# Kernel optimization log

Hardware: AMD Instinct MI355X
Metric: run time of the kernel (lower is better)

## Reference

```python
import jax, jax.numpy as jnp
import numpy as np

IN_C, OUT_C, K, PAD = 4, 32, 5, 2
B, H, W = 128, 84, 84
T_MAX = 15.0
BASE_THR = 15.0
TARGET_RATE = 0.05
LR_PLUS, LR_MINUS = 0.004, 0.0012
HOMEO, EMA_DECAY = 0.01, 0.99
FAN_IN_SQRT = float((IN_C * K * K) ** 0.5)


def setup_inputs() -> dict:
    key = jax.random.key(0)
    k1, k2, k3 = jax.random.split(key, 3)
    lat = jax.random.uniform(k1, (B, IN_C, H, W), jnp.float32, 0.0, T_MAX)
    lat = lat * (jax.random.uniform(k3, (B, IN_C, H, W)) > 0.3).astype(jnp.float32)
    w = jax.random.uniform(k2, (OUT_C, IN_C, K, K)) * 0.6 + 0.2
    norm = jnp.linalg.norm(w.reshape(OUT_C, -1), axis=1).reshape(-1, 1, 1, 1)
    w = w / (norm + 1e-6) * FAN_IN_SQRT
    thr = jnp.full((OUT_C,), BASE_THR, jnp.float32)
    ema = jnp.full((OUT_C,), TARGET_RATE, jnp.float32)
    return {"spike_latencies": lat, "weight": w, "adaptive_threshold": thr, "firing_rate_ema": ema}


def reference(spike_latencies, weight, adaptive_threshold, firing_rate_ema):
    # is_training_stdp=True path: returns (out_latencies, new_weight, new_threshold, new_ema)
    active = (spike_latencies > 0).astype(spike_latencies.dtype)   # (B,Cin,H,W)
    pot_in = (T_MAX - spike_latencies) * active
    pot_out = jax.lax.conv_general_dilated(
        pot_in, weight, (1, 1), [(PAD, PAD), (PAD, PAD)],
        dimension_numbers=("NCHW", "OIHW", "NCHW"))                # (B,Cout,H,W)

    winners = jnp.argmax(pot_out, axis=1)                           # (B,H,W)
    max_pot = jnp.max(pot_out, axis=1)                              # (B,H,W)
    win_thr = adaptive_threshold[winners]                           # (B,H,W)
    fire = (max_pot >= win_thr).astype(pot_out.dtype)               # (B,H,W)
    out_spikes = jax.nn.one_hot(winners, OUT_C, axis=1, dtype=pot_out.dtype) * fire[:, None]

    winners_flat = winners.reshape(-1)                              # (N,) N = B*H*W
    fire_flat = fire.reshape(-1)

    # ---- homeostatic threshold update (no_grad in torch) ----
    count = jax.ops.segment_sum(fire_flat, winners_flat, num_segments=OUT_C)  # fires per channel
    spatial_count = float(B * H * W)
    cur_rate = count / (spatial_count + 1e-8)
    new_ema = EMA_DECAY * firing_rate_ema + (1.0 - EMA_DECAY) * cur_rate
    rate_err = new_ema - TARGET_RATE
    new_thr = jnp.clip(adaptive_threshold + HOMEO * rate_err * adaptive_threshold,
                       BASE_THR * 0.1, BASE_THR * 5.0)

    # ---- STDP weight update (no_grad in torch) ----
    # im2col of the binary activity map; feature dim is ordered (Cin, K, K)
    patches = jax.lax.conv_general_dilated_patches(
        active, (K, K), (1, 1), [(PAD, PAD), (PAD, PAD)])           # (B, Cin*K*K, H, W)
    patches = patches.transpose(0, 2, 3, 1).reshape(-1, IN_C, K, K)  # (N,Cin,K,K)

    # sum of pre-activity patches per winning channel, masked by fire
    S_pre = jax.ops.segment_sum(patches * fire_flat[:, None, None, None],
                                winners_flat, num_segments=OUT_C)    # (Cout,Cin,K,K)

    fired = count > 0
    # min/max over the gathered winner weights == min/max over channels that fired
    ch_min = weight.min(axis=(1, 2, 3))
    ch_max = weight.max(axis=(1, 2, 3))
    w_min = jnp.min(jnp.where(fired, ch_min, jnp.inf))
    w_max = jnp.max(jnp.where(fired, ch_max, -jnp.inf))
    w_normed = (weight - w_min) / (w_max - w_min + 1e-6)

    # sum over fired positions of per-position delta, closed form per channel
    cnt = count[:, None, None, None]
    total_delta = LR_PLUS * (1.0 - w_normed) * S_pre - LR_MINUS * w_normed * (cnt - S_pre)
    total_delta = jnp.where(fired[:, None, None, None],
                            total_delta / jnp.maximum(cnt, 1.0), 0.0)

    w_upd = jnp.maximum(weight + total_delta, 0.01)
    norm = jnp.linalg.norm(w_upd.reshape(OUT_C, -1), axis=1).reshape(-1, 1, 1, 1)
    w_upd = w_upd / (norm + 1e-6) * FAN_IN_SQRT
    new_weight = jnp.where(jnp.any(fired), w_upd, weight)

    out_latencies = (T_MAX * BASE_THR / (max_pot + 1e-5))[:, None] * out_spikes  # (B,Cout,H,W)
    return out_latencies, new_weight, new_thr, new_ema
```

## Files before the change

### kernel.cpp

```cpp
#include <hip/hip_runtime.h>
#include <hip/hip_bf16.h>

#define H_ 84
#define W_ 84
#define B_ 128
#define ICN 4
#define OCN 32
#define HW (H_*W_)
#define OUT_LAT (B_*OCN*HW)
#define OUT_WOFF OUT_LAT
#define OUT_THROFF (OUT_WOFF + 3200)
#define OUT_EMAOFF (OUT_WOFF + 3232)

#define WF_OFF   0
#define SPRE_OFF 903168
#define CNT_OFF  (SPRE_OFF + 12800)
#define LCNT_OFF (CNT_OFF + 128)
#define W4T_OFF  (LCNT_OFF + 128)
#define LIST_OFF (W4T_OFF + 12800)
#define LIST_CAP 32768
#define PART_OFF (LIST_OFF + LIST_CAP*4)
#define NSLAB 7
#define NBLK (B_*NSLAB)
#define LREDN 3232

__global__ __launch_bounds__(256) void wtrans_kernel(const float* __restrict__ w,
                                                     float* __restrict__ w4t) {
  int i = blockIdx.x * 256 + threadIdx.x;
  if (i < 3200) {
    int c = i / 100, r = i % 100, ic = r / 25, t = r % 25;
    w4t[(t * 32 + c) * 4 + ic] = w[i];
  }
}

__global__ __launch_bounds__(256, 4) void conv_kernel(const float* __restrict__ lat,
    const float* __restrict__ w4t, const float* __restrict__ thr,
    float* __restrict__ out, unsigned char* __restrict__ wfmap,
    unsigned* __restrict__ lcnt, unsigned* __restrict__ list) {
  __shared__ float4 tile[20][20];
  const int b = blockIdx.z;
  const int bx = blockIdx.x * 16, by = blockIdx.y * 16;
  const int tid = threadIdx.y * 16 + threadIdx.x;
  const float* base = lat + (size_t)b * ICN * HW;
  for (int n = tid; n < 400; n += 256) {
    int iy = n / 20, ix = n % 20;
    int gy = by + iy - 2, gx = bx + ix - 2;
    float4 v = make_float4(0.f, 0.f, 0.f, 0.f);
    if (gy >= 0 && gy < H_ && gx >= 0 && gx < W_) {
      const float* p = base + gy * W_ + gx;
      float a0 = p[0], a1 = p[HW], a2 = p[2 * HW], a3 = p[3 * HW];
      v.x = a0 > 0.f ? 15.0f - a0 : 0.f;
      v.y = a1 > 0.f ? 15.0f - a1 : 0.f;
      v.z = a2 > 0.f ? 15.0f - a2 : 0.f;
      v.w = a3 > 0.f ? 15.0f - a3 : 0.f;
    }
    tile[iy][ix] = v;
  }
  __syncthreads();
  const int x = bx + threadIdx.x, y = by + threadIdx.y;
  if (x >= W_ || y >= H_) return;
  const float4* w4 = (const float4*)w4t;
  float s[32];
  #pragma unroll
  for (int c = 0; c < 32; c++) s[c] = 0.f;
  for (int i = 0; i < 5; i++) {
    for (int j = 0; j < 5; j++) {
      float4 pv = tile[threadIdx.y + i][threadIdx.x + j];
      int t = i * 5 + j;
      #pragma unroll
      for (int c = 0; c < 32; c++) {
        float4 wv = w4[t * 32 + c];
        s[c] = fmaf(pv.x, wv.x, s[c]);
        s[c] = fmaf(pv.y, wv.y, s[c]);
        s[c] = fmaf(pv.z, wv.z, s[c]);
        s[c] = fmaf(pv.w, wv.w, s[c]);
      }
    }
  }
  float best = s[0], second = -__builtin_inff();
  int bc = 0, bc2 = 0;
  #pragma unroll
  for (int c = 1; c < 32; c++) {
    float v = s[c];
    if (v > best) { second = best; bc2 = bc; best = v; bc = c; }
    else if (v > second) { second = v; bc2 = c; }
  }
  float tb = thr[bc];
  bool fire = best >= tb;
  float latv = 225.0f / (best + 1e-5f);
  bool risky_gap = (best - second) < 0.02f;
  bool risky_thr = fabsf(best - tb) < 0.02f;
  bool need_exact = risky_thr || (risky_gap && latv >= 0.55f);
  bool deferred = false;
  if (need_exact) {
    unsigned idx = atomicAdd(lcnt, 1u);
    if (idx < LIST_CAP) { list[idx] = (unsigned)(b * HW + y * W_ + x); deferred = true; }
  }
  if (!deferred) {
    bool split = risky_gap && !need_exact;
    wfmap[b * HW + y * W_ + x] = (unsigned char)(bc | (fire ? 0x80 : 0));
    if (fire) {
      size_t o = (size_t)b * OCN * HW + (size_t)y * W_ + x;
      if (split) {
        float h = 0.5f * latv;
        out[o + (size_t)bc  * HW] = h;
        out[o + (size_t)bc2 * HW] = h;
      } else {
        out[o + (size_t)bc * HW] = latv;
      }
    }
  }
}

__global__ __launch_bounds__(256, 2) void repair_kernel(const float* __restrict__ lat,
    const float* __restrict__ weight, const float* __restrict__ thr,
    float* __restrict__ out, unsigned char* __restrict__ wfmap,
    const unsigned* __restrict__ lcnt, const unsigned* __restrict__ list) {
  unsigned n = *lcnt;
  if (n > LIST_CAP) n = LIST_CAP;
  for (unsigned i = blockIdx.x * 256 + threadIdx.x; i < n; i += gridDim.x * 256) {
    unsigned pix = list[i];
    int b = (int)(pix / HW), r = (int)(pix % HW);
    int y = r / W_, x = r % W_;
    const float* base = lat + (size_t)b * ICN * HW;
    float raw[100];
    #pragma unroll
    for (int ic = 0; ic < 4; ic++)
      #pragma unroll
      for (int kh = 0; kh < 5; kh++)
        #pragma unroll
        for (int kw = 0; kw < 5; kw++) {
          int gy = y + kh - 2, gx = x + kw - 2;
          raw[ic * 25 + kh * 5 + kw] =
            (gy >= 0 && gy < H_ && gx >= 0 && gx < W_) ? base[ic * HW + gy * W_ + gx] : 0.f;
        }
    double dbest = -1.0e300;
    int bc = 0;
    for (int c = 0; c < 32; c++) {
      const float* wr = weight + c * 100;
      double s = 0.0;
      for (int q = 0; q < 100; q++) {
        float a = raw[q];
        double pot = a > 0.f ? 15.0 - (double)a : 0.0;
        s += pot * (double)wr[q];
      }
      if (s > dbest) { dbest = s; bc = c; }
    }
    bool fire = dbest >= (double)thr[bc];
    wfmap[pix] = (unsigned char)(bc | (fire ? 0x80 : 0));
    if (fire)
      out[((size_t)b * OCN + bc) * HW + (size_t)y * W_ + x] = (float)(225.0 / (dbest + 1e-5));
  }
}

__device__ __forceinline__ unsigned long long winshift(unsigned long long lo,
                                                       unsigned long long hi, int s) {
  if (s < 0)  return lo << (-s);
  if (s == 0) return lo;
  if (s < 64) return (lo >> s) | (hi << (64 - s));
  return hi >> (s - 64);
}

__global__ __launch_bounds__(256, 4) void spre_kernel(const float* __restrict__ lat,
    const unsigned char* __restrict__ wfmap,
    unsigned* __restrict__ spre, unsigned* __restrict__ cnt,
    unsigned* __restrict__ partial) {
  __shared__ unsigned arow[16][ICN][3];
  __shared__ unsigned lred[LREDN];
  const int b = blockIdx.x;
  const int y0 = blockIdx.y * 12;
  const int tid = threadIdx.x;
  const int wv = tid >> 6, lane = tid & 63;
  for (int i = tid; i < LREDN; i += 256) lred[i] = 0;
  #pragma unroll
  for (int i = 0; i < 16; i++) {
    int pair = wv * 16 + i;
    int r = pair >> 2, ic = pair & 3;
    int gy = y0 - 2 + r;
    unsigned w0 = 0, w1 = 0, w2 = 0;
    if (gy >= 0 && gy < H_) {
      const float* rp = lat + ((size_t)b * ICN + ic) * HW + gy * W_;
      unsigned long long mA = __ballot(rp[lane] > 0.f);
      float vB = (lane < 20) ? rp[64 + lane] : 0.f;
      unsigned long long mB = __ballot(vB > 0.f);
      w0 = (unsigned)mA; w1 = (unsigned)(mA >> 32); w2 = (unsigned)mB;
    }
    if (lane == 0) { arow[r][ic][0] = w0; arow[r][ic][1] = w1; arow[r][ic][2] = w2; }
  }
  __syncthreads();
  unsigned acc0[16], acc1[16];
  #pragma unroll
  for (int c = 0; c < 16; c++) { acc0[c] = 0; acc1[c] = 0; }
  for (int k = 0; k < 6; k++) {
    int task = k * 4 + wv;
    int y = y0 + (task >> 1);
    int grp = task & 1;
    int xbase = grp * 64;
    bool valid = (grp == 0) || (lane < 20);
    unsigned wf = valid ? (unsigned)wfmap[b * HW + y * W_ + xbase + lane] : 0u;
    bool f = valid && (wf & 0x80u);
    int wc = (int)(wf & 31u);
    unsigned long long win0, win1;
    {
      int q = lane;
      int ic = q / 25, rr = q % 25, kh = rr / 5, kw = rr % 5;
      int ry = (y - y0) + kh;
      unsigned a0 = arow[ry][ic][0], a1 = arow[ry][ic][1], a2 = arow[ry][ic][2];
      unsigned long long lo = ((unsigned long long)a1 << 32) | a0;
      unsigned long long hi = a2;
      win0 = winshift(lo, hi, xbase + kw - 2);
      if (lane < 36) {
        q = 64 + lane;
        ic = q / 25; rr = q % 25; kh = rr / 5; kw = rr % 5;
        ry = (y - y0) + kh;
        a0 = arow[ry][ic][0]; a1 = arow[ry][ic][1]; a2 = arow[ry][ic][2];
        lo = ((unsigned long long)a1 << 32) | a0; hi = a2;
        win1 = winshift(lo, hi, xbase + kw - 2);
      } else if (lane == 36) {
        win1 = grp ? ((1ull << 20) - 1) : ~0ull;
      } else {
        win1 = 0ull;
      }
    }
    #pragma unroll
    for (int cc = 0; cc < 16; cc++) {
      unsigned long long m0 = __ballot(f && (wc == cc));
      unsigned long long m1 = __ballot(f && (wc == 16 + cc));
      acc0[cc] += (unsigned)__popcll(win0 & m0) | ((unsigned)__popcll(win0 & m1) << 16);
      acc1[cc] += (unsigned)__popcll(win1 & m0) | ((unsigned)__popcll(win1 & m1) << 16);
    }
  }
  #pragma unroll
  for (int cc = 0; cc < 16; cc++) {
    atomicAdd(&lred[cc * 101 + lane], acc0[cc] & 0xFFFFu);
    atomicAdd(&lred[(cc + 16) * 101 + lane], acc0[cc] >> 16);
    if (lane <= 36) {
      int q = (lane < 36) ? 64 + lane : 100;
      atomicAdd(&lred[cc * 101 + q], acc1[cc] & 0xFFFFu);
      atomicAdd(&lred[(cc + 16) * 101 + q], acc1[cc] >> 16);
    }
  }
  __syncthreads();
  if (partial) {
    unsigned bflat = (unsigned)(blockIdx.x * NSLAB + blockIdx.y);
    for (int i = tid; i < LREDN; i += 256)
      partial[bflat * LREDN + i] = lred[i];
  } else {
    for (int i = tid; i < LREDN; i += 256) {
      unsigned v = lred[i];
      if (v) {
        int c = i / 101, q = i % 101;
        if (q < 100) atomicAdd(&spre[c * 100 + q], v);
        else         atomicAdd(&cnt[c], v);
      }
    }
  }
}

__global__ __launch_bounds__(256) void reduce_kernel(const unsigned* __restrict__ partial,
    unsigned* __restrict__ spre, unsigned* __restrict__ cnt) {
  int i = blockIdx.x * 256 + threadIdx.x;
  if (i >= LREDN) return;
  unsigned s = 0;
  for (int j = 0; j < NBLK; j++) s += partial[(size_t)j * LREDN + i];
  int c = i / 101, q = i % 101;
  if (q < 100) spre[c * 100 + q] = s;
  else         cnt[c] = s;
}

__global__ void finalize_kernel(const float* __restrict__ weight, const float* __restrict__ thr,
    const float* __restrict__ ema, const unsigned* __restrict__ spre,
    const unsigned* __restrict__ cnt, float* __restrict__ out) {
  int lane = threadIdx.x;
  int c = lane & 31;
  bool hold = lane < 32;
  unsigned cu = cnt[c];
  float cntf = (float)cu;
  bool fired = cu > 0u;
  float emaN = 0.99f * ema[c] + 0.01f * (cntf / (903168.0f + 1e-8f));
  float thrN = thr[c] + 0.01f * (emaN - 0.05f) * thr[c];
  thrN = fminf(fmaxf(thrN, 1.5f), 75.0f);
  float chmin = __builtin_inff(), chmax = -__builtin_inff();
  for (int j = 0; j < 100; j++) {
    float w = weight[c * 100 + j];
    chmin = fminf(chmin, w); chmax = fmaxf(chmax, w);
  }
  float vmin = (hold && fired) ? chmin : __builtin_inff();
  float vmax = (hold && fired) ? chmax : -__builtin_inff();
  #pragma unroll
  for (int o = 1; o < 64; o <<= 1) {
    vmin = fminf(vmin, __shfl_xor(vmin, o));
    vmax = fmaxf(vmax, __shfl_xor(vmax, o));
  }
  bool any = __ballot(hold && fired) != 0ull;
  float denom = vmax - vmin + 1e-6f;
  float invc = 1.0f / fmaxf(cntf, 1.0f);
  float sumsq = 0.f;
  for (int j = 0; j < 100; j++) {
    float w = weight[c * 100 + j];
    float wn = (w - vmin) / denom;
    float sp = (float)spre[c * 100 + j];
    float d = 0.004f * (1.0f - wn) * sp - 0.0012f * wn * (cntf - sp);
    d = fired ? d * invc : 0.0f;
    float wu = fmaxf(w + d, 0.01f);
    sumsq += wu * wu;
  }
  float scale = 10.0f / (sqrtf(sumsq) + 1e-6f);
  if (hold) {
    for (int j = 0; j < 100; j++) {
      float w = weight[c * 100 + j];
      float wn = (w - vmin) / denom;
      float sp = (float)spre[c * 100 + j];
      float d = 0.004f * (1.0f - wn) * sp - 0.0012f * wn * (cntf - sp);
      d = fired ? d * invc : 0.0f;
      float wu = fmaxf(w + d, 0.01f);
      out[OUT_WOFF + c * 100 + j] = any ? wu * scale : w;
    }
    out[OUT_THROFF + c] = thrN;
    out[OUT_EMAOFF + c] = emaN;
  }
}

extern "C" void kernel_launch(void* const* d_in, const int* in_sizes, int n_in,
                              void* d_out, int out_size, void* d_ws, size_t ws_size,
                              hipStream_t stream) {
  (void)in_sizes; (void)n_in; (void)out_size;
  const float* lat    = (const float*)d_in[0];
  const float* weight = (const float*)d_in[1];
  const float* thr    = (const float*)d_in[2];
  const float* ema    = (const float*)d_in[3];
  float* out = (float*)d_out;
  char* ws = (char*)d_ws;
  unsigned char* wfmap = (unsigned char*)(ws + WF_OFF);
  unsigned* spre = (unsigned*)(ws + SPRE_OFF);
  unsigned* cnt  = (unsigned*)(ws + CNT_OFF);
  unsigned* lcnt = (unsigned*)(ws + LCNT_OFF);
  float* w4t     = (float*)(ws + W4T_OFF);
  unsigned* list = (unsigned*)(ws + LIST_OFF);
  unsigned* part = (unsigned*)(ws + PART_OFF);
  bool useP = ws_size >= (size_t)PART_OFF + (size_t)NBLK * LREDN * 4;

  hipMemsetAsync(d_out, 0, (size_t)OUT_LAT * 4, stream);
  hipMemsetAsync(ws + SPRE_OFF, 0, 12800 + 256, stream);
  wtrans_kernel<<<13, 256, 0, stream>>>(weight, w4t);
  conv_kernel<<<dim3(6, 6, B_), dim3(16, 16, 1), 0, stream>>>(lat, w4t, thr, out, wfmap, lcnt, list);
  repair_kernel<<<64, 256, 0, stream>>>(lat, weight, thr, out, wfmap, lcnt, list);
  spre_kernel<<<dim3(B_, NSLAB), 256, 0, stream>>>(lat, wfmap, spre, cnt, useP ? part : nullptr);
  if (useP) reduce_kernel<<<(LREDN + 255) / 256, 256, 0, stream>>>(part, spre, cnt);
  finalize_kernel<<<1, 64, 0, stream>>>(weight, thr, ema, spre, cnt, out);
}
```

Measured before the change: 275.4 us.

## Cache input patch in registers and loop over output channels with streaming argmax

Reorders the convolution loops so each thread loads its 5x5x4 input patch from shared memory into registers once. It then iterates over output channels, computing one dot product at a time and updating the running top-two argmax as it goes, instead of keeping 32 accumulators live. The transposed weights are re-laid out channel-major to match this order, and the shared tile row is padded to 21 to reduce bank conflicts. The cost is about 100 VGPRs for the patch and long serial FMA chains with only 2-way channel unrolling, which risks spills or less latency hiding under the 256x4 launch bounds.

```diff
diff --git a/kernel.cpp b/kernel.cpp
--- a/kernel.cpp
+++ b/kernel.cpp
@@ -29,7 +29,7 @@
   int i = blockIdx.x * 256 + threadIdx.x;
   if (i < 3200) {
     int c = i / 100, r = i % 100, ic = r / 25, t = r % 25;
-    w4t[(t * 32 + c) * 4 + ic] = w[i];
+    w4t[(c * 25 + t) * 4 + ic] = w[i];
   }
 }
 
@@ -37,7 +37,7 @@
     const float* __restrict__ w4t, const float* __restrict__ thr,
     float* __restrict__ out, unsigned char* __restrict__ wfmap,
     unsigned* __restrict__ lcnt, unsigned* __restrict__ list) {
-  __shared__ float4 tile[20][20];
+  __shared__ float4 tile[20][21];
   const int b = blockIdx.z;
   const int bx = blockIdx.x * 16, by = blockIdx.y * 16;
   const int tid = threadIdx.y * 16 + threadIdx.x;
@@ -59,31 +59,29 @@
   __syncthreads();
   const int x = bx + threadIdx.x, y = by + threadIdx.y;
   if (x >= W_ || y >= H_) return;
+  float4 p[25];
+  #pragma unroll
+  for (int i = 0; i < 5; i++)
+    #pragma unroll
+    for (int j = 0; j < 5; j++)
+      p[i * 5 + j] = tile[threadIdx.y + i][threadIdx.x + j];
   const float4* w4 = (const float4*)w4t;
-  float s[32];
-  #pragma unroll
-  for (int c = 0; c < 32; c++) s[c] = 0.f;
-  for (int i = 0; i < 5; i++) {
-    for (int j = 0; j < 5; j++) {
-      float4 pv = tile[threadIdx.y + i][threadIdx.x + j];
-      int t = i * 5 + j;
-      #pragma unroll
-      for (int c = 0; c < 32; c++) {
-        float4 wv = w4[t * 32 + c];
-        s[c] = fmaf(pv.x, wv.x, s[c]);
-        s[c] = fmaf(pv.y, wv.y, s[c]);
-        s[c] = fmaf(pv.z, wv.z, s[c]);
-        s[c] = fmaf(pv.w, wv.w, s[c]);
-      }
-    }
-  }
-  float best = s[0], second = -__builtin_inff();
+  float best = -__builtin_inff(), second = -__builtin_inff();
   int bc = 0, bc2 = 0;
-  #pragma unroll
-  for (int c = 1; c < 32; c++) {
-    float v = s[c];
-    if (v > best) { second = best; bc2 = bc; best = v; bc = c; }
-    else if (v > second) { second = v; bc2 = c; }
+  #pragma unroll 2
+  for (int c = 0; c < 32; c++) {
+    const float4* wc = w4 + c * 25;
+    float s = 0.f;
+    #pragma unroll
+    for (int t = 0; t < 25; t++) {
+      float4 wv = wc[t];
+      s = fmaf(p[t].x, wv.x, s);
+      s = fmaf(p[t].y, wv.y, s);
+      s = fmaf(p[t].z, wv.z, s);
+      s = fmaf(p[t].w, wv.w, s);
+    }
+    if (s > best) { second = best; bc2 = bc; best = s; bc = c; }
+    else if (s > second) { second = s; bc2 = c; }
   }
   float tb = thr[bc];
   bool fire = best >= tb;
```

New measurement: 293.9 us. 1.07x slower.
